# Kernel optimization log

Measured on AMD Instinct MI355X. Metric: run time of the kernel, lower is better.

## Reference

```python
import jax, jax.numpy as jnp
import numpy as np

IN_CH = 63      # positionally-encoded points
IN_VIEWS = 63   # positionally-encoded view dirs (must equal IN_CH per source bug)
UNITS = 256
N = 131072
SKIPS = (4,)


def _linear_init(key, fan_in, fan_out):
    # torch nn.Linear default: U(-1/sqrt(fan_in), 1/sqrt(fan_in)) for W and b
    kw, kb = jax.random.split(key)
    bound = 1.0 / np.sqrt(fan_in)
    W = jax.random.uniform(kw, (fan_in, fan_out), jnp.float32, -bound, bound)
    b = jax.random.uniform(kb, (fan_out,), jnp.float32, -bound, bound)
    return W, b


def setup_inputs() -> dict:
    key = jax.random.key(0)
    keys = jax.random.split(key, 16)
    inp = {}
    inp["x"] = jax.random.normal(keys[0], (N, IN_CH + IN_VIEWS), jnp.float32)
    # 8 backbone layers; layer idx 5 consumes skip-concat of width UNITS+IN_CH
    fan_ins = [IN_CH] + [UNITS + IN_CH if (i - 1) in SKIPS else UNITS for i in range(1, 8)]
    for i, fi in enumerate(fan_ins):
        W, b = _linear_init(keys[1 + i], fi, UNITS)
        inp[f"W{i}"], inp[f"b{i}"] = W, b
    inp["Wf"], inp["bf"] = _linear_init(keys[9], UNITS, UNITS)          # linear_feature
    inp["Wa"], inp["ba"] = _linear_init(keys[10], UNITS, 1)             # linear_alpha
    inp["Wv"], inp["bv"] = _linear_init(keys[11], IN_CH + UNITS, UNITS // 2)  # linear_views[0]
    inp["Wr"], inp["br"] = _linear_init(keys[12], UNITS // 2, 3)        # linear_rgb
    return inp


def reference(x, W0, b0, W1, b1, W2, b2, W3, b3, W4, b4, W5, b5, W6, b6, W7, b7,
              Wf, bf, Wa, ba, Wv, bv, Wr, br):
    pts = x[..., :IN_CH]
    views = x[..., IN_CH:]
    Ws = (W0, W1, W2, W3, W4, W5, W6, W7)
    bs = (b0, b1, b2, b3, b4, b5, b6, b7)
    h = pts
    for idx in range(8):
        h = jax.nn.relu(h @ Ws[idx] + bs[idx])
        if idx in SKIPS:
            h = jnp.concatenate([pts, h], axis=-1)  # [N, IN_CH + UNITS]
    alpha = h @ Wa + ba                       # [N, 1]
    feature = h @ Wf + bf                     # [N, UNITS]
    hv = jnp.concatenate([feature, views], axis=-1)   # [N, UNITS + IN_VIEWS]
    hv = jax.nn.relu(hv @ Wv + bv)            # [N, UNITS//2]
    rgb = hv @ Wr + br                        # [N, 3]
    return jnp.concatenate([rgb, alpha], axis=-1)     # [N, 4]
```

## Files before the change

kernel.cpp:

```cpp
#include <hip/hip_runtime.h>
#include <hip/hip_bf16.h>


typedef __bf16 bfrag __attribute__((ext_vector_type(8)));
typedef float  f4    __attribute__((ext_vector_type(4)));
typedef unsigned short us4 __attribute__((ext_vector_type(4)));

constexpr int OFF_W0 = 0;
constexpr int OFF_W1 = 16384;
constexpr int OFF_W2 = 81920;
constexpr int OFF_W3 = 147456;
constexpr int OFF_W4 = 212992;
constexpr int OFF_W5 = 278528;
constexpr int OFF_W6 = 360448;
constexpr int OFF_W7 = 425984;
constexpr int OFF_WF = 491520;
constexpr int OFF_WV = 557056;
constexpr int OFF_WA = 598016;
constexpr int OFF_WR = 602112;
constexpr int WS_TOTAL = 604160;

__device__ __forceinline__ unsigned swz256(int row, int k) {
  return (unsigned)((row * 256 + k) ^ ((row & 7) << 3));
}
__device__ __forceinline__ unsigned swz64(int row, int k) {
  return (unsigned)((row * 64 + k) ^ ((row & 7) << 3));
}

template<int NCT, int NKS, int NCTS, int SSTR>
__device__ __forceinline__ void phase(f4 (&acc)[4][NCT],
    const unsigned short* __restrict__ src,
    const unsigned short* __restrict__ wt, int ks0, int ctb,
    int lane, int l15, int lk8) {
#pragma unroll
  for (int ks = 0; ks < NKS; ++ks) {
    const int kl = ks * 32 + lk8;
    bfrag a[4];
#pragma unroll
    for (int rt = 0; rt < 4; ++rt) {
      const unsigned idx = (SSTR == 256) ? swz256(rt * 16 + l15, kl)
                                         : swz64(rt * 16 + l15, kl);
      a[rt] = *(const bfrag*)(src + idx);
    }
    const unsigned short* wk =
        wt + ((size_t)(ks0 + ks) * NCTS + ctb) * 512 + lane * 8;
    constexpr int CH = (NCT < 4) ? NCT : 4;
#pragma unroll
    for (int c2 = 0; c2 < NCT; c2 += CH) {
      bfrag b[CH];
#pragma unroll
      for (int u = 0; u < CH; ++u)
        b[u] = *(const bfrag*)(wk + (size_t)(c2 + u) * 512);
#pragma unroll
      for (int u = 0; u < CH; ++u)
#pragma unroll
        for (int rt = 0; rt < 4; ++rt)
          acc[rt][c2 + u] = __builtin_amdgcn_mfma_f32_16x16x32_bf16(b[u], a[rt], acc[rt][c2 + u], 0, 0, 0);
    }
  }
}

template<int NCT>
__device__ __forceinline__ void init_acc(f4 (&acc)[4][NCT],
    const float* __restrict__ bias, int cb, int lk4) {
#pragma unroll
  for (int ct = 0; ct < NCT; ++ct) {
    const float4 bv = *(const float4*)(bias + cb + ct * 16 + lk4);
    f4 v = {bv.x, bv.y, bv.z, bv.w};
#pragma unroll
    for (int rt = 0; rt < 4; ++rt) acc[rt][ct] = v;
  }
}

template<bool RELU, int NCT>
__device__ __forceinline__ void store_h(f4 (&acc)[4][NCT],
    unsigned short* __restrict__ h, int cb, int l15, int lk4) {
#pragma unroll
  for (int ct = 0; ct < NCT; ++ct) {
    const int col0 = cb + ct * 16 + lk4;
#pragma unroll
    for (int rt = 0; rt < 4; ++rt) {
      us4 packed;
#pragma unroll
      for (int j = 0; j < 4; ++j) {
        float v = acc[rt][ct][j];
        if (RELU) v = fmaxf(v, 0.f);
        __bf16 bb = (__bf16)v;
        packed[j] = __builtin_bit_cast(unsigned short, bb);
      }
      *(us4*)(h + swz256(rt * 16 + l15, col0)) = packed;
    }
  }
}

__device__ __forceinline__ void stage_inputs(const float* __restrict__ x,
    unsigned short* pts, unsigned short* views, int rowg0, int tid) {
  const int row = tid >> 2, seg = tid & 3;
  const float* xr = x + (size_t)(rowg0 + row) * 126;
  bfrag v0, v1;
#pragma unroll
  for (int q = 0; q < 4; ++q) {
    const int c = seg * 16 + 2 * q;
    float2 t = *(const float2*)(xr + c);
    v0[2 * q]     = (c     < 63) ? (__bf16)t.x : (__bf16)0.f;
    v0[2 * q + 1] = (c + 1 < 63) ? (__bf16)t.y : (__bf16)0.f;
  }
#pragma unroll
  for (int q = 0; q < 4; ++q) {
    const int c = seg * 16 + 8 + 2 * q;
    float2 t = *(const float2*)(xr + c);
    v1[2 * q]     = (c     < 63) ? (__bf16)t.x : (__bf16)0.f;
    v1[2 * q + 1] = (c + 1 < 63) ? (__bf16)t.y : (__bf16)0.f;
  }
  *(bfrag*)(pts + swz64(row, seg * 16))     = v0;
  *(bfrag*)(pts + swz64(row, seg * 16 + 8)) = v1;
  bfrag w0, w1;
#pragma unroll
  for (int j = 0; j < 8; ++j) {
    const int c = seg * 16 + j;
    w0[j] = (c < 63) ? (__bf16)xr[63 + c] : (__bf16)0.f;
  }
#pragma unroll
  for (int j = 0; j < 8; ++j) {
    const int c = seg * 16 + 8 + j;
    w1[j] = (c < 63) ? (__bf16)xr[63 + c] : (__bf16)0.f;
  }
  *(bfrag*)(views + swz64(row, seg * 16))     = w0;
  *(bfrag*)(views + swz64(row, seg * 16 + 8)) = w1;
}

struct RepackArgs {
  const float *W0, *W1, *W2, *W3, *W4, *W5, *W6, *W7, *Wf, *Wv, *Wa, *Wr;
  unsigned short* ws;
};

__global__ void repack_kernel(RepackArgs a) {
  const int i = blockIdx.x * 256 + threadIdx.x;
  if (i >= WS_TOTAL) return;

  const float* src; int off, ncts, fanin, fanout; bool shift = false;
  int mode = 0;
  if      (i < OFF_W1) { src = a.W0; off = OFF_W0; ncts = 16; fanin = 63;  fanout = 256; }
  else if (i < OFF_W2) { src = a.W1; off = OFF_W1; ncts = 16; fanin = 256; fanout = 256; }
  else if (i < OFF_W3) { src = a.W2; off = OFF_W2; ncts = 16; fanin = 256; fanout = 256; }
  else if (i < OFF_W4) { src = a.W3; off = OFF_W3; ncts = 16; fanin = 256; fanout = 256; }
  else if (i < OFF_W5) { src = a.W4; off = OFF_W4; ncts = 16; fanin = 256; fanout = 256; }
  else if (i < OFF_W6) { src = a.W5; off = OFF_W5; ncts = 16; fanin = 319; fanout = 256; shift = true; }
  else if (i < OFF_W7) { src = a.W6; off = OFF_W6; ncts = 16; fanin = 256; fanout = 256; }
  else if (i < OFF_WF) { src = a.W7; off = OFF_W7; ncts = 16; fanin = 256; fanout = 256; }
  else if (i < OFF_WV) { src = a.Wf; off = OFF_WF; ncts = 16; fanin = 256; fanout = 256; }
  else if (i < OFF_WA) { src = a.Wv; off = OFF_WV; ncts = 8;  fanin = 319; fanout = 128; }
  else if (i < OFF_WR) { src = a.Wa; off = OFF_WA; ncts = 1;  fanin = 256; fanout = 1; mode = 1; }
  else                 { src = a.Wr; off = OFF_WR; ncts = 1;  fanin = 128; fanout = 3; mode = 2; }

  const int idx  = i - off;
  const int j    = idx & 7;
  const int lane = (idx >> 3) & 63;
  const int rem  = idx >> 9;
  const int ctg  = rem % ncts;
  const int ks   = rem / ncts;
  const int k    = ks * 32 + ((lane >> 4) << 3) + j;
  const int col  = ctg * 16 + (lane & 15);

  float v;
  if (mode == 1) {
    v = (col == 0 && k < fanin) ? src[k] : 0.f;
  } else if (mode == 2) {
    v = (col < 3 && k < fanin) ? src[(size_t)k * 3 + col] : 0.f;
  } else if (shift) {
    v = (k < 63) ? src[(size_t)k * 256 + col]
                 : ((k == 63) ? 0.f : src[(size_t)(k - 1) * 256 + col]);
  } else {
    v = (k < fanin) ? src[(size_t)k * fanout + col] : 0.f;
  }
  __bf16 bb = (__bf16)v;
  a.ws[i] = __builtin_bit_cast(unsigned short, bb);
}

struct MainArgs {
  const float* x;
  const unsigned short* ws;
  const float *b0, *b1, *b2, *b3, *b4, *b5, *b6, *b7;
  const float *bfc, *ba, *bv, *br;
  float* out;
};

__global__ __launch_bounds__(256, 2) void nerf_kernel(MainArgs A) {
  extern __shared__ unsigned short lds[];
  unsigned short* hA    = lds;
  unsigned short* hB    = lds + 64 * 256;
  unsigned short* pts   = lds + 2 * 64 * 256;
  unsigned short* views = pts + 64 * 64;

  const int tid  = threadIdx.x;
  const int lane = tid & 63;
  const int wave = tid >> 6;
  const int l15 = lane & 15;
  const int lk8 = (lane >> 4) << 3;
  const int lk4 = (lane >> 4) << 2;
  const int cb  = wave * 64;
  const int ctb = wave * 4;
  const int rowg0 = blockIdx.x * 64;
  const unsigned short* ws = A.ws;

  stage_inputs(A.x, pts, views, rowg0, tid);
  __syncthreads();

  f4 acc[4][4];

  init_acc<4>(acc, A.b0, cb, lk4);
  phase<4, 2, 16, 64>(acc, pts, ws + OFF_W0, 0, ctb, lane, l15, lk8);
  store_h<true, 4>(acc, hA, cb, l15, lk4);
  __syncthreads();

  init_acc<4>(acc, A.b1, cb, lk4);
  phase<4, 8, 16, 256>(acc, hA, ws + OFF_W1, 0, ctb, lane, l15, lk8);
  store_h<true, 4>(acc, hB, cb, l15, lk4);
  __syncthreads();

  init_acc<4>(acc, A.b2, cb, lk4);
  phase<4, 8, 16, 256>(acc, hB, ws + OFF_W2, 0, ctb, lane, l15, lk8);
  store_h<true, 4>(acc, hA, cb, l15, lk4);
  __syncthreads();

  init_acc<4>(acc, A.b3, cb, lk4);
  phase<4, 8, 16, 256>(acc, hA, ws + OFF_W3, 0, ctb, lane, l15, lk8);
  store_h<true, 4>(acc, hB, cb, l15, lk4);
  __syncthreads();

  init_acc<4>(acc, A.b4, cb, lk4);
  phase<4, 8, 16, 256>(acc, hB, ws + OFF_W4, 0, ctb, lane, l15, lk8);
  store_h<true, 4>(acc, hA, cb, l15, lk4);
  __syncthreads();

  init_acc<4>(acc, A.b5, cb, lk4);
  phase<4, 2, 16, 64>(acc, pts, ws + OFF_W5, 0, ctb, lane, l15, lk8);
  phase<4, 8, 16, 256>(acc, hA, ws + OFF_W5, 2, ctb, lane, l15, lk8);
  store_h<true, 4>(acc, hB, cb, l15, lk4);
  __syncthreads();

  init_acc<4>(acc, A.b6, cb, lk4);
  phase<4, 8, 16, 256>(acc, hB, ws + OFF_W6, 0, ctb, lane, l15, lk8);
  store_h<true, 4>(acc, hA, cb, l15, lk4);
  __syncthreads();

  init_acc<4>(acc, A.b7, cb, lk4);
  phase<4, 8, 16, 256>(acc, hA, ws + OFF_W7, 0, ctb, lane, l15, lk8);
  store_h<true, 4>(acc, hB, cb, l15, lk4);
  __syncthreads();

  if (wave == 0) {
    f4 accA[4][1];
#pragma unroll
    for (int rt = 0; rt < 4; ++rt) accA[rt][0] = (f4){0.f, 0.f, 0.f, 0.f};
    phase<1, 8, 1, 256>(accA, hB, ws + OFF_WA, 0, 0, lane, l15, lk8);
    if (lk4 == 0) {
      const float ba0 = A.ba[0];
#pragma unroll
      for (int rt = 0; rt < 4; ++rt)
        A.out[(size_t)(rowg0 + rt * 16 + l15) * 4 + 3] = accA[rt][0][0] + ba0;
    }
  }

  init_acc<4>(acc, A.bfc, cb, lk4);
  phase<4, 8, 16, 256>(acc, hB, ws + OFF_WF, 0, ctb, lane, l15, lk8);
  store_h<false, 4>(acc, hA, cb, l15, lk4);
  __syncthreads();

  {
    f4 acc2[4][2];
    const int cb2 = wave * 32;
    init_acc<2>(acc2, A.bv, cb2, lk4);
    phase<2, 8, 8, 256>(acc2, hA, ws + OFF_WV, 0, wave * 2, lane, l15, lk8);
    phase<2, 2, 8, 64>(acc2, views, ws + OFF_WV, 8, wave * 2, lane, l15, lk8);
    store_h<true, 2>(acc2, hB, cb2, l15, lk4);
  }
  __syncthreads();

  if (wave == 0) {
    f4 accR[4][1];
#pragma unroll
    for (int rt = 0; rt < 4; ++rt) accR[rt][0] = (f4){0.f, 0.f, 0.f, 0.f};
    phase<1, 4, 1, 256>(accR, hB, ws + OFF_WR, 0, 0, lane, l15, lk8);
    if (lk4 == 0) {
#pragma unroll
      for (int rt = 0; rt < 4; ++rt) {
        float* o = A.out + (size_t)(rowg0 + rt * 16 + l15) * 4;
#pragma unroll
        for (int j = 0; j < 3; ++j) o[j] = accR[rt][0][j] + A.br[j];
      }
    }
  }
}

extern "C" void kernel_launch(void* const* d_in, const int* in_sizes, int n_in,
                              void* d_out, int out_size, void* d_ws, size_t ws_size,
                              hipStream_t stream) {
  RepackArgs ra;
  ra.W0 = (const float*)d_in[1];  ra.W1 = (const float*)d_in[3];
  ra.W2 = (const float*)d_in[5];  ra.W3 = (const float*)d_in[7];
  ra.W4 = (const float*)d_in[9];  ra.W5 = (const float*)d_in[11];
  ra.W6 = (const float*)d_in[13]; ra.W7 = (const float*)d_in[15];
  ra.Wf = (const float*)d_in[17]; ra.Wv = (const float*)d_in[21];
  ra.Wa = (const float*)d_in[19]; ra.Wr = (const float*)d_in[23];
  ra.ws = (unsigned short*)d_ws;
  repack_kernel<<<(WS_TOTAL + 255) / 256, 256, 0, stream>>>(ra);

  MainArgs ma;
  ma.x   = (const float*)d_in[0];
  ma.ws  = (const unsigned short*)d_ws;
  ma.b0  = (const float*)d_in[2];  ma.b1 = (const float*)d_in[4];
  ma.b2  = (const float*)d_in[6];  ma.b3 = (const float*)d_in[8];
  ma.b4  = (const float*)d_in[10]; ma.b5 = (const float*)d_in[12];
  ma.b6  = (const float*)d_in[14]; ma.b7 = (const float*)d_in[16];
  ma.bfc = (const float*)d_in[18];
  ma.ba  = (const float*)d_in[20];
  ma.bv  = (const float*)d_in[22];
  ma.br  = (const float*)d_in[24];
  ma.out = (float*)d_out;

  const int n    = in_sizes[0] / 126;
  const int grid = n / 64;

  hipFuncSetAttribute(reinterpret_cast<const void*>(nerf_kernel),
                      hipFuncAttributeMaxDynamicSharedMemorySize, 81920);
  nerf_kernel<<<grid, 256, 81920, stream>>>(ma);
}
```

Measured before the change: 167.3 us.

## Double rows per block with 8 waves and share pts/views LDS buffer

Each block now processes 128 rows with 512 threads arranged as 2 row-groups × 4 column-groups, instead of 64 rows with 256 threads. Points and view encodings now share one LDS buffer: views are staged after the skip layer has consumed the points. This cuts the LDS footprint per row, and blocks that share a CU may reuse weight fetches through cache. In exchange, barriers now span 8 waves, and the 144KB of LDS allows only one block per CU. `__launch_bounds__(512,2)` also caps registers per thread more tightly, which risks spills.

```diff
diff --git a/kernel.cpp b/kernel.cpp
--- a/kernel.cpp
+++ b/kernel.cpp
@@ -30,7 +30,7 @@
 template<int NCT, int NKS, int NCTS, int SSTR>
 __device__ __forceinline__ void phase(f4 (&acc)[4][NCT],
     const unsigned short* __restrict__ src,
-    const unsigned short* __restrict__ wt, int ks0, int ctb,
+    const unsigned short* __restrict__ wt, int ks0, int ctb, int r0,
     int lane, int l15, int lk8) {
 #pragma unroll
   for (int ks = 0; ks < NKS; ++ks) {
@@ -38,8 +38,8 @@
     bfrag a[4];
 #pragma unroll
     for (int rt = 0; rt < 4; ++rt) {
-      const unsigned idx = (SSTR == 256) ? swz256(rt * 16 + l15, kl)
-                                         : swz64(rt * 16 + l15, kl);
+      const int row = r0 + rt * 16 + l15;
+      const unsigned idx = (SSTR == 256) ? swz256(row, kl) : swz64(row, kl);
       a[rt] = *(const bfrag*)(src + idx);
     }
     const unsigned short* wk =
@@ -74,7 +74,7 @@
 
 template<bool RELU, int NCT>
 __device__ __forceinline__ void store_h(f4 (&acc)[4][NCT],
-    unsigned short* __restrict__ h, int cb, int l15, int lk4) {
+    unsigned short* __restrict__ h, int cb, int r0, int l15, int lk4) {
 #pragma unroll
   for (int ct = 0; ct < NCT; ++ct) {
     const int col0 = cb + ct * 16 + lk4;
@@ -88,13 +88,13 @@
         __bf16 bb = (__bf16)v;
         packed[j] = __builtin_bit_cast(unsigned short, bb);
       }
-      *(us4*)(h + swz256(rt * 16 + l15, col0)) = packed;
-    }
-  }
-}
-
-__device__ __forceinline__ void stage_inputs(const float* __restrict__ x,
-    unsigned short* pts, unsigned short* views, int rowg0, int tid) {
+      *(us4*)(h + swz256(r0 + rt * 16 + l15, col0)) = packed;
+    }
+  }
+}
+
+__device__ __forceinline__ void stage_pts(const float* __restrict__ x,
+    unsigned short* pv, int rowg0, int tid) {
   const int row = tid >> 2, seg = tid & 3;
   const float* xr = x + (size_t)(rowg0 + row) * 126;
   bfrag v0, v1;
@@ -112,21 +112,27 @@
     v1[2 * q]     = (c     < 63) ? (__bf16)t.x : (__bf16)0.f;
     v1[2 * q + 1] = (c + 1 < 63) ? (__bf16)t.y : (__bf16)0.f;
   }
-  *(bfrag*)(pts + swz64(row, seg * 16))     = v0;
-  *(bfrag*)(pts + swz64(row, seg * 16 + 8)) = v1;
+  *(bfrag*)(pv + swz64(row, seg * 16))     = v0;
+  *(bfrag*)(pv + swz64(row, seg * 16 + 8)) = v1;
+}
+
+__device__ __forceinline__ void stage_views(const float* __restrict__ x,
+    unsigned short* pv, int rowg0, int tid) {
+  const int row = tid >> 2, seg = tid & 3;
+  const float* xr = x + (size_t)(rowg0 + row) * 126 + 63;
   bfrag w0, w1;
 #pragma unroll
   for (int j = 0; j < 8; ++j) {
     const int c = seg * 16 + j;
-    w0[j] = (c < 63) ? (__bf16)xr[63 + c] : (__bf16)0.f;
+    w0[j] = (c < 63) ? (__bf16)xr[c] : (__bf16)0.f;
   }
 #pragma unroll
   for (int j = 0; j < 8; ++j) {
     const int c = seg * 16 + 8 + j;
-    w1[j] = (c < 63) ? (__bf16)xr[63 + c] : (__bf16)0.f;
-  }
-  *(bfrag*)(views + swz64(row, seg * 16))     = w0;
-  *(bfrag*)(views + swz64(row, seg * 16 + 8)) = w1;
+    w1[j] = (c < 63) ? (__bf16)xr[c] : (__bf16)0.f;
+  }
+  *(bfrag*)(pv + swz64(row, seg * 16))     = w0;
+  *(bfrag*)(pv + swz64(row, seg * 16 + 8)) = w1;
 }
 
 struct RepackArgs {
@@ -185,107 +191,111 @@
   float* out;
 };
 
-__global__ __launch_bounds__(256, 2) void nerf_kernel(MainArgs A) {
+__global__ __launch_bounds__(512, 2) void nerf_kernel(MainArgs A) {
   extern __shared__ unsigned short lds[];
-  unsigned short* hA    = lds;
-  unsigned short* hB    = lds + 64 * 256;
-  unsigned short* pts   = lds + 2 * 64 * 256;
-  unsigned short* views = pts + 64 * 64;
+  unsigned short* hA = lds;
+  unsigned short* hB = lds + 128 * 256;
+  unsigned short* pv = lds + 2 * 128 * 256;
 
   const int tid  = threadIdx.x;
   const int lane = tid & 63;
   const int wave = tid >> 6;
+  const int wr   = wave >> 2;
+  const int wc   = wave & 3;
   const int l15 = lane & 15;
   const int lk8 = (lane >> 4) << 3;
   const int lk4 = (lane >> 4) << 2;
-  const int cb  = wave * 64;
-  const int ctb = wave * 4;
-  const int rowg0 = blockIdx.x * 64;
+  const int r0  = wr * 64;
+  const int cb  = wc * 64;
+  const int ctb = wc * 4;
+  const int rowg0 = blockIdx.x * 128;
   const unsigned short* ws = A.ws;
 
-  stage_inputs(A.x, pts, views, rowg0, tid);
+  stage_pts(A.x, pv, rowg0, tid);
   __syncthreads();
 
   f4 acc[4][4];
 
   init_acc<4>(acc, A.b0, cb, lk4);
-  phase<4, 2, 16, 64>(acc, pts, ws + OFF_W0, 0, ctb, lane, l15, lk8);
-  store_h<true, 4>(acc, hA, cb, l15, lk4);
+  phase<4, 2, 16, 64>(acc, pv, ws + OFF_W0, 0, ctb, r0, lane, l15, lk8);
+  store_h<true, 4>(acc, hA, cb, r0, l15, lk4);
   __syncthreads();
 
   init_acc<4>(acc, A.b1, cb, lk4);
-  phase<4, 8, 16, 256>(acc, hA, ws + OFF_W1, 0, ctb, lane, l15, lk8);
-  store_h<true, 4>(acc, hB, cb, l15, lk4);
+  phase<4, 8, 16, 256>(acc, hA, ws + OFF_W1, 0, ctb, r0, lane, l15, lk8);
+  store_h<true, 4>(acc, hB, cb, r0, l15, lk4);
   __syncthreads();
 
   init_acc<4>(acc, A.b2, cb, lk4);
-  phase<4, 8, 16, 256>(acc, hB, ws + OFF_W2, 0, ctb, lane, l15, lk8);
-  store_h<true, 4>(acc, hA, cb, l15, lk4);
+  phase<4, 8, 16, 256>(acc, hB, ws + OFF_W2, 0, ctb, r0, lane, l15, lk8);
+  store_h<true, 4>(acc, hA, cb, r0, l15, lk4);
   __syncthreads();
 
   init_acc<4>(acc, A.b3, cb, lk4);
-  phase<4, 8, 16, 256>(acc, hA, ws + OFF_W3, 0, ctb, lane, l15, lk8);
-  store_h<true, 4>(acc, hB, cb, l15, lk4);
+  phase<4, 8, 16, 256>(acc, hA, ws + OFF_W3, 0, ctb, r0, lane, l15, lk8);
+  store_h<true, 4>(acc, hB, cb, r0, l15, lk4);
   __syncthreads();
 
   init_acc<4>(acc, A.b4, cb, lk4);
-  phase<4, 8, 16, 256>(acc, hB, ws + OFF_W4, 0, ctb, lane, l15, lk8);
-  store_h<true, 4>(acc, hA, cb, l15, lk4);
+  phase<4, 8, 16, 256>(acc, hB, ws + OFF_W4, 0, ctb, r0, lane, l15, lk8);
+  store_h<true, 4>(acc, hA, cb, r0, l15, lk4);
   __syncthreads();
 
   init_acc<4>(acc, A.b5, cb, lk4);
-  phase<4, 2, 16, 64>(acc, pts, ws + OFF_W5, 0, ctb, lane, l15, lk8);
-  phase<4, 8, 16, 256>(acc, hA, ws + OFF_W5, 2, ctb, lane, l15, lk8);
-  store_h<true, 4>(acc, hB, cb, l15, lk4);
-  __syncthreads();
+  phase<4, 2, 16, 64>(acc, pv, ws + OFF_W5, 0, ctb, r0, lane, l15, lk8);
+  phase<4, 8, 16, 256>(acc, hA, ws + OFF_W5, 2, ctb, r0, lane, l15, lk8);
+  store_h<true, 4>(acc, hB, cb, r0, l15, lk4);
+  __syncthreads();
+
+  stage_views(A.x, pv, rowg0, tid);
 
   init_acc<4>(acc, A.b6, cb, lk4);
-  phase<4, 8, 16, 256>(acc, hB, ws + OFF_W6, 0, ctb, lane, l15, lk8);
-  store_h<true, 4>(acc, hA, cb, l15, lk4);
+  phase<4, 8, 16, 256>(acc, hB, ws + OFF_W6, 0, ctb, r0, lane, l15, lk8);
+  store_h<true, 4>(acc, hA, cb, r0, l15, lk4);
   __syncthreads();
 
   init_acc<4>(acc, A.b7, cb, lk4);
-  phase<4, 8, 16, 256>(acc, hA, ws + OFF_W7, 0, ctb, lane, l15, lk8);
-  store_h<true, 4>(acc, hB, cb, l15, lk4);
-  __syncthreads();
-
-  if (wave == 0) {
+  phase<4, 8, 16, 256>(acc, hA, ws + OFF_W7, 0, ctb, r0, lane, l15, lk8);
+  store_h<true, 4>(acc, hB, cb, r0, l15, lk4);
+  __syncthreads();
+
+  if (wc == 0) {
     f4 accA[4][1];
 #pragma unroll
     for (int rt = 0; rt < 4; ++rt) accA[rt][0] = (f4){0.f, 0.f, 0.f, 0.f};
-    phase<1, 8, 1, 256>(accA, hB, ws + OFF_WA, 0, 0, lane, l15, lk8);
+    phase<1, 8, 1, 256>(accA, hB, ws + OFF_WA, 0, 0, r0, lane, l15, lk8);
     if (lk4 == 0) {
       const float ba0 = A.ba[0];
 #pragma unroll
       for (int rt = 0; rt < 4; ++rt)
-        A.out[(size_t)(rowg0 + rt * 16 + l15) * 4 + 3] = accA[rt][0][0] + ba0;
+        A.out[(size_t)(rowg0 + r0 + rt * 16 + l15) * 4 + 3] = accA[rt][0][0] + ba0;
     }
   }
 
   init_acc<4>(acc, A.bfc, cb, lk4);
-  phase<4, 8, 16, 256>(acc, hB, ws + OFF_WF, 0, ctb, lane, l15, lk8);
-  store_h<false, 4>(acc, hA, cb, l15, lk4);
+  phase<4, 8, 16, 256>(acc, hB, ws + OFF_WF, 0, ctb, r0, lane, l15, lk8);
+  store_h<false, 4>(acc, hA, cb, r0, l15, lk4);
   __syncthreads();
 
   {
     f4 acc2[4][2];
-    const int cb2 = wave * 32;
+    const int cb2 = wc * 32;
     init_acc<2>(acc2, A.bv, cb2, lk4);
-    phase<2, 8, 8, 256>(acc2, hA, ws + OFF_WV, 0, wave * 2, lane, l15, lk8);
-    phase<2, 2, 8, 64>(acc2, views, ws + OFF_WV, 8, wave * 2, lane, l15, lk8);
-    store_h<true, 2>(acc2, hB, cb2, l15, lk4);
-  }
-  __syncthreads();
-
-  if (wave == 0) {
+    phase<2, 8, 8, 256>(acc2, hA, ws + OFF_WV, 0, wc * 2, r0, lane, l15, lk8);
+    phase<2, 2, 8, 64>(acc2, pv, ws + OFF_WV, 8, wc * 2, r0, lane, l15, lk8);
+    store_h<true, 2>(acc2, hB, cb2, r0, l15, lk4);
+  }
+  __syncthreads();
+
+  if (wc == 0) {
     f4 accR[4][1];
 #pragma unroll
     for (int rt = 0; rt < 4; ++rt) accR[rt][0] = (f4){0.f, 0.f, 0.f, 0.f};
-    phase<1, 4, 1, 256>(accR, hB, ws + OFF_WR, 0, 0, lane, l15, lk8);
+    phase<1, 4, 1, 256>(accR, hB, ws + OFF_WR, 0, 0, r0, lane, l15, lk8);
     if (lk4 == 0) {
 #pragma unroll
       for (int rt = 0; rt < 4; ++rt) {
-        float* o = A.out + (size_t)(rowg0 + rt * 16 + l15) * 4;
+        float* o = A.out + (size_t)(rowg0 + r0 + rt * 16 + l15) * 4;
 #pragma unroll
         for (int j = 0; j < 3; ++j) o[j] = accR[rt][0][j] + A.br[j];
       }
@@ -320,9 +330,9 @@
   ma.out = (float*)d_out;
 
   const int n    = in_sizes[0] / 126;
-  const int grid = n / 64;
+  const int grid = n / 128;
 
   hipFuncSetAttribute(reinterpret_cast<const void*>(nerf_kernel),
-                      hipFuncAttributeMaxDynamicSharedMemorySize, 81920);
-  nerf_kernel<<<grid, 256, 81920, stream>>>(ma);
-}
+                      hipFuncAttributeMaxDynamicSharedMemorySize, 147456);
+  nerf_kernel<<<grid, 512, 147456, stream>>>(ma);
+}
```

Result: slower. 199.9 us (+19.5%).
